# Optimization experiments

Measured on AMD Instinct MI355X. Metric: run time of the kernel, lower is better.

The kernel has to match this reference:

```python
import jax, jax.numpy as jnp
import numpy as np

D_MODEL = 1024
NUM_HEADS = 16
D_K = D_MODEL // NUM_HEADS
MAX_SEQ_LEN = 2048
THETA = 10000.0


def setup_inputs() -> dict:
    key = jax.random.key(0)
    k0, k1, k2, k3, k4 = jax.random.split(key, 5)
    B, S = 2, 2048
    std = (2.0 / (D_MODEL + D_MODEL)) ** 0.5
    # trunc_normal with std=std*std approximated by normal scaled (same distributional scale)
    w = lambda k: (std * std) * jax.random.truncated_normal(k, -3.0 / std, 3.0 / std, (D_MODEL, D_MODEL), jnp.float32)
    return {
        "in_features": jax.random.normal(k0, (B, S, D_MODEL), jnp.float32),
        "token_positions": jnp.arange(S, dtype=jnp.int32),
        "Wq": w(k1), "Wk": w(k2), "Wv": w(k3), "Wo": w(k4),
    }


def _rope(x, token_positions):
    # x: [B, H, S, d_k]; interleaved even/odd rotation
    freq = 1.0 / jnp.power(THETA, jnp.arange(0, D_K, 2, dtype=jnp.float32) / D_K)
    pos = jnp.arange(MAX_SEQ_LEN, dtype=jnp.float32)
    freqs = jnp.outer(pos, freq)                      # [max_seq, d_k/2]
    cos = jnp.cos(freqs)[token_positions]             # [S, d_k/2]
    sin = jnp.sin(freqs)[token_positions]
    even, odd = x[..., 0::2], x[..., 1::2]
    even_out = even * cos - odd * sin
    odd_out = even * sin + odd * cos
    return jnp.stack([even_out, odd_out], axis=-1).reshape(x.shape)


def reference(in_features, token_positions, Wq, Wk, Wv, Wo):
    B, S, _ = in_features.shape
    split = lambda t: t.reshape(B, S, NUM_HEADS, D_K).transpose(0, 2, 1, 3)  # [B,H,S,d_k]
    q = split(in_features @ Wq.T)
    k = split(in_features @ Wk.T)
    v = split(in_features @ Wv.T)
    q = _rope(q, token_positions)
    k = _rope(k, token_positions)
    score = jnp.einsum('bhqd,bhkd->bhqk', q, k) / jnp.sqrt(jnp.float32(D_K))
    mask = jnp.tril(jnp.ones((S, S), dtype=bool))
    score = jnp.where(mask, score, -jnp.inf)
    attn = jax.nn.softmax(score, axis=-1)
    out = jnp.einsum('bhqk,bhkd->bhqd', attn, v)       # [B,H,S,d_k]
    out = out.transpose(0, 2, 1, 3).reshape(B, S, D_MODEL)
    return out @ Wo.T
```

## Files before the change

kernel.cpp:

```cpp
#include <hip/hip_runtime.h>
#include <stdint.h>


typedef unsigned short u16;
typedef __bf16 bf16x8 __attribute__((ext_vector_type(8)));
typedef float f32x4 __attribute__((ext_vector_type(4)));
typedef u16 u16x4 __attribute__((ext_vector_type(4)));

#define LOG2E 1.44269504088896340736f
#define QSCALE (0.125f * LOG2E)

static __device__ __forceinline__ u16 f2bf(float f) {
  __bf16 b = (__bf16)f;
  return __builtin_bit_cast(u16, b);
}

extern "C" __device__ float __ocml_native_exp2_f32(float);
static __device__ __forceinline__ float fexp2(float x) {
#if __has_builtin(__builtin_amdgcn_exp2f)
  return __builtin_amdgcn_exp2f(x);
#else
  return __ocml_native_exp2_f32(x);
#endif
}

template<bool F32>
static __device__ __forceinline__ bf16x8 load8(const void* p, size_t off) {
  if constexpr (F32) {
    const float* f = (const float*)p + off;
    f32x4 a = *(const f32x4*)f;
    f32x4 b = *(const f32x4*)(f + 4);
    bf16x8 r;
    r[0] = (__bf16)a[0]; r[1] = (__bf16)a[1]; r[2] = (__bf16)a[2]; r[3] = (__bf16)a[3];
    r[4] = (__bf16)b[0]; r[5] = (__bf16)b[1]; r[6] = (__bf16)b[2]; r[7] = (__bf16)b[3];
    return r;
  } else {
    return *(const bf16x8*)((const u16*)p + off);
  }
}

static __device__ __forceinline__ void glds16(const u16* g, u16* l) {
  __builtin_amdgcn_global_load_lds(
      (const __attribute__((address_space(1))) unsigned int*)g,
      (__attribute__((address_space(3))) unsigned int*)l, 16, 0, 0);
}

__global__ void prep_kernel(const float* __restrict__ Wq, const float* __restrict__ Wk,
                            const float* __restrict__ Wv, const float* __restrict__ Wo,
                            u16* __restrict__ wout,
                            const float* __restrict__ x, u16* __restrict__ xout,
                            size_t xn8,
                            const int* __restrict__ tp,
                            float* __restrict__ cosT, float* __restrict__ sinT) {
  const int z = blockIdx.z;
  const int i = blockIdx.x * 256 + threadIdx.x;
  if (z == 4) {
    if (i >= 2048 * 32) return;
    int s = i >> 5, fi = i & 31;
    float p = (float)tp[s];
    float freq = powf(10000.0f, -(float)fi / 32.0f);
    float ang = p * freq;
    cosT[i] = cosf(ang);
    sinT[i] = sinf(ang);
    return;
  }
  const float* src;
  u16* dst;
  size_t off;
  if (z < 4) {
    if (i >= 1024 * 1024 / 8) return;
    src = (z == 0) ? Wq : (z == 1) ? Wk : (z == 2) ? Wv : Wo;
    dst = wout + (size_t)z * 1024 * 1024;
    off = (size_t)i * 8;
  } else {
    size_t gi = (size_t)(z - 5) * (512 * 256) + i;
    if (gi >= xn8) return;
    src = x;
    dst = xout;
    off = gi * 8;
  }
  const float* p = src + off;
  f32x4 a = *(const f32x4*)p;
  f32x4 b = *(const f32x4*)(p + 4);
  bf16x8 r;
  r[0] = (__bf16)a[0]; r[1] = (__bf16)a[1]; r[2] = (__bf16)a[2]; r[3] = (__bf16)a[3];
  r[4] = (__bf16)b[0]; r[5] = (__bf16)b[1]; r[6] = (__bf16)b[2]; r[7] = (__bf16)b[3];
  *(bf16x8*)(dst + off) = r;
}

template<bool AF32, bool BF32>
static __device__ __forceinline__ void gemm128_core(
    const void* __restrict__ A, const void* __restrict__ W,
    u16* As, u16* Bs, int m0, int n0, f32x4 (&acc)[4][4]) {
  const int tid = threadIdx.x;
  const int lane = tid & 63;
  const int wave = tid >> 6;
  const int wr = (wave >> 1) * 64, wc = (wave & 1) * 64;
  const int lr = lane & 15, lg = lane >> 4;
  const int srow = tid >> 3;
  const int scol = ((tid & 7) ^ (srow & 7)) * 8;
  for (int k0 = 0; k0 < 1024; k0 += 64) {
    if constexpr (!AF32 && !BF32) {
      const u16* Ab = (const u16*)A;
      const u16* Wb = (const u16*)W;
      __syncthreads();
#pragma unroll
      for (int i = 0; i < 4; ++i) {
        glds16(Ab + (size_t)(m0 + srow + i * 32) * 1024 + k0 + scol, As + tid * 8 + i * 2048);
        glds16(Wb + (size_t)(n0 + srow + i * 32) * 1024 + k0 + scol, Bs + tid * 8 + i * 2048);
      }
      __syncthreads();
    } else {
      bf16x8 ta[4], tb[4];
#pragma unroll
      for (int i = 0; i < 4; ++i) {
        ta[i] = load8<AF32>(A, (size_t)(m0 + srow + i * 32) * 1024 + k0 + scol);
        tb[i] = load8<BF32>(W, (size_t)(n0 + srow + i * 32) * 1024 + k0 + scol);
      }
      __syncthreads();
#pragma unroll
      for (int i = 0; i < 4; ++i) {
        *(bf16x8*)(As + tid * 8 + i * 2048) = ta[i];
        *(bf16x8*)(Bs + tid * 8 + i * 2048) = tb[i];
      }
      __syncthreads();
    }
#pragma unroll
    for (int kk = 0; kk < 2; ++kk) {
      bf16x8 af[4], bfr[4];
#pragma unroll
      for (int i = 0; i < 4; ++i) {
        const int ga = ((kk * 4 + lg) ^ (lr & 7)) * 8;
        af[i]  = *(const bf16x8*)(As + (wr + i * 16 + lr) * 64 + ga);
        bfr[i] = *(const bf16x8*)(Bs + (wc + i * 16 + lr) * 64 + ga);
      }
#pragma unroll
      for (int i = 0; i < 4; ++i)
#pragma unroll
        for (int j = 0; j < 4; ++j)
          acc[i][j] = __builtin_amdgcn_mfma_f32_16x16x32_bf16(af[i], bfr[j], acc[i][j], 0, 0, 0);
    }
  }
}

template<bool F32>
__global__ __launch_bounds__(256, 3)
void qkv_gemm_kernel(const void* __restrict__ X,
                     const void* __restrict__ Wq, const void* __restrict__ Wk,
                     const void* __restrict__ Wv,
                     const float* __restrict__ cosT, const float* __restrict__ sinT,
                     u16* __restrict__ Qo, u16* __restrict__ Ko, u16* __restrict__ Vto) {
  __shared__ __align__(16) u16 As[128 * 64];
  __shared__ __align__(16) u16 Bs[128 * 64];
  const int z = blockIdx.z;
  const void* W = (z == 0) ? Wq : ((z == 1) ? Wk : Wv);
  const int m0 = blockIdx.x * 128, n0 = blockIdx.y * 128;
  f32x4 acc[4][4] = {};
  gemm128_core<F32, F32>(X, W, As, Bs, m0, n0, acc);
  const int lane = threadIdx.x & 63, wave = threadIdx.x >> 6;
  const int wr = (wave >> 1) * 64, wc = (wave & 1) * 64;
  const int lr = lane & 15, lg = lane >> 4;
  if (z < 2) {
    u16* dst = z ? Ko : Qo;
    const float qs = z ? 1.0f : QSCALE;
    const int parity = lr & 1;
#pragma unroll
    for (int i = 0; i < 4; ++i) {
      const int rb = m0 + wr + i * 16 + lg * 4;
#pragma unroll
      for (int n = 0; n < 4; ++n) {
        const int c = n0 + wc + n * 16 + lr;
        const int hh = c >> 6, d = c & 63;
        const int ifr = d >> 1;
#pragma unroll
        for (int j = 0; j < 4; ++j) {
          const int r = rb + j;
          const int s = r & 2047;
          float v = acc[i][n][j];
          float p = __shfl_xor(v, 1);
          float cs = cosT[s * 32 + ifr];
          float sn = sinT[s * 32 + ifr];
          float res = parity ? (p * sn + v * cs) : (v * cs - p * sn);
          dst[(((size_t)(r >> 11) * 16 + hh) * 2048 + s) * 64 + d] =
              f2bf(res * qs);
        }
      }
    }
  } else {
#pragma unroll
    for (int i = 0; i < 4; ++i) {
      const int s0 = m0 + wr + i * 16 + lg * 4;
      const int bb = s0 >> 11, ss = s0 & 2047;
#pragma unroll
      for (int n = 0; n < 4; ++n) {
        const int c = n0 + wc + n * 16 + lr;
        const int hh = c >> 6, d = c & 63;
        u16x4 pk;
#pragma unroll
        for (int j = 0; j < 4; ++j) pk[j] = f2bf(acc[i][n][j]);
        *(u16x4*)(Vto + (((size_t)bb * 16 + hh) * 64 + d) * 2048 + ss) = pk;
      }
    }
  }
}

template<bool MASKED>
static __device__ __forceinline__ void attn_tile(
    const u16* kb, const u16* vb, int kv0, int qrow,
    const bf16x8 (&qf)[2], u16* Psw,
    f32x4 (&accO)[4], float& m, float& l, int lr, int lg) {
  f32x4 sacc[4] = {};
  __builtin_amdgcn_s_setprio(1);
#pragma unroll
  for (int n = 0; n < 4; ++n)
#pragma unroll
    for (int kk = 0; kk < 2; ++kk) {
      const int gsw = ((((kk << 2) | lg) ^ (lr & 7)) << 3);
      bf16x8 kf = *(const bf16x8*)&kb[(n * 16 + lr) * 64 + gsw];
      sacc[n] = __builtin_amdgcn_mfma_f32_16x16x32_bf16(kf, qf[kk], sacc[n], 0, 0, 0);
    }
  __builtin_amdgcn_s_setprio(0);
  if (MASKED) {
#pragma unroll
    for (int n = 0; n < 4; ++n)
#pragma unroll
      for (int j = 0; j < 4; ++j) {
        const int c = kv0 + n * 16 + lg * 4 + j;
        if (c > qrow) sacc[n][j] = -1e30f;
      }
  }
  float t0 = fmaxf(fmaxf(sacc[0][0], sacc[0][1]), sacc[0][2]);
  float t1 = fmaxf(fmaxf(sacc[0][3], sacc[1][0]), sacc[1][1]);
  float t2 = fmaxf(fmaxf(sacc[1][2], sacc[1][3]), sacc[2][0]);
  float t3 = fmaxf(fmaxf(sacc[2][1], sacc[2][2]), sacc[2][3]);
  float t4 = fmaxf(fmaxf(sacc[3][0], sacc[3][1]), sacc[3][2]);
  float tm = fmaxf(fmaxf(t0, t1), fmaxf(fmaxf(t2, t3), fmaxf(t4, sacc[3][3])));
  tm = fmaxf(tm, __shfl_xor(tm, 16));
  tm = fmaxf(tm, __shfl_xor(tm, 32));

  float ssum = 0.f;
  u16x4 pk[4];
  if (__all(tm <= m + 8.0f)) {
#pragma unroll
    for (int n = 0; n < 4; ++n)
#pragma unroll
      for (int j = 0; j < 4; ++j) {
        float p = fexp2(sacc[n][j] - m);
        ssum += p;
        pk[n][j] = f2bf(p);
      }
    ssum += __shfl_xor(ssum, 16);
    ssum += __shfl_xor(ssum, 32);
    l += ssum;
  } else {
    const float mn = fmaxf(m, tm);
    const float al = fexp2(m - mn);
    m = mn;
#pragma unroll
    for (int n = 0; n < 4; ++n)
#pragma unroll
      for (int j = 0; j < 4; ++j) {
        float p = fexp2(sacc[n][j] - mn);
        ssum += p;
        pk[n][j] = f2bf(p);
      }
    ssum += __shfl_xor(ssum, 16);
    ssum += __shfl_xor(ssum, 32);
    l = l * al + ssum;
#pragma unroll
    for (int n = 0; n < 4; ++n)
#pragma unroll
      for (int j = 0; j < 4; ++j)
        accO[n][j] *= al;
  }
#pragma unroll
  for (int n = 0; n < 4; ++n) {
    const int g = n * 4 + lg;
    const int off = ((((g >> 1) ^ (lr & 7)) << 3) | ((g & 1) << 2));
    *(u16x4*)&Psw[lr * 64 + off] = pk[n];
  }
  __builtin_amdgcn_s_setprio(1);
#pragma unroll
  for (int kk = 0; kk < 2; ++kk) {
    const int po = (((kk * 4 + lg) ^ (lr & 7)) << 3);
    bf16x8 pb = *(const bf16x8*)&Psw[lr * 64 + po];
#pragma unroll
    for (int db = 0; db < 4; ++db) {
      const int gsw = ((((kk << 2) | lg) ^ (lr & 7)) << 3);
      bf16x8 vf = *(const bf16x8*)&vb[(db * 16 + lr) * 64 + gsw];
      accO[db] = __builtin_amdgcn_mfma_f32_16x16x32_bf16(vf, pb, accO[db], 0, 0, 0);
    }
  }
  __builtin_amdgcn_s_setprio(0);
}

__global__ __launch_bounds__(256, 4)
void flash_attn_kernel(const u16* __restrict__ Q, const u16* __restrict__ K,
                       const u16* __restrict__ Vt, u16* __restrict__ O) {
  __shared__ __align__(16) u16 Klds[2][64 * 64];
  __shared__ __align__(16) u16 Vlds[2][64 * 64];
  __shared__ __align__(16) u16 Ps[4][16 * 64];
  const int bh = blockIdx.x;
  const int qcb = 31 - (int)blockIdx.y;
  const int b = bh >> 4, h = bh & 15;
  const int tid = threadIdx.x;
  const int wv = tid >> 6, lane = tid & 63;
  const int lr = lane & 15, lg = lane >> 4;
  const int qbase = qcb * 64 + wv * 16;
  const int qrow = qbase + lr;
  const size_t hb = (size_t)bh * (2048 * 64);
  const u16* Qh = Q + hb;

  const int sgr = ((lane & 7) ^ (lane >> 3)) << 3;
  const int srw = lane >> 3;
  const u16* kp = K + hb + (size_t)(wv * 16 + srw) * 64 + sgr;
  const u16* vp = Vt + hb + (size_t)(wv * 16 + srw) * 2048 + sgr;
  const int ldso = (wv * 16) * 64;
  auto STAGE = [&](const u16* kq, const u16* vq, int bufi) {
    u16* kbd = Klds[bufi] + ldso;
    u16* vbd = Vlds[bufi] + ldso;
    glds16(kq, kbd);
    glds16(kq + 8 * 64, kbd + 8 * 64);
    glds16(vq, vbd);
    glds16(vq + 8 * 2048, vbd + 8 * 64);
  };

  bf16x8 qf[2];
#pragma unroll
  for (int kk = 0; kk < 2; ++kk)
    qf[kk] = *(const bf16x8*)(Qh + (size_t)qrow * 64 + kk * 32 + lg * 8);

  f32x4 accO[4] = {};
  float m = -1e30f, l = 0.f;

  const int nt = qcb + 1;
  STAGE(kp, vp, 0);
  kp += 64 * 64; vp += 64;
  __syncthreads();
  for (int t = 0; t < nt - 1; ++t) {
    STAGE(kp, vp, (t & 1) ^ 1);
    kp += 64 * 64; vp += 64;
    attn_tile<false>(Klds[t & 1], Vlds[t & 1], t * 64, qrow, qf, Ps[wv],
                     accO, m, l, lr, lg);
    __syncthreads();
  }
  attn_tile<true>(Klds[(nt - 1) & 1], Vlds[(nt - 1) & 1], (nt - 1) * 64, qrow,
                  qf, Ps[wv], accO, m, l, lr, lg);

  const float inv = 1.0f / l;
#pragma unroll
  for (int db = 0; db < 4; ++db) {
    u16x4 pk;
#pragma unroll
    for (int j = 0; j < 4; ++j) pk[j] = f2bf(accO[db][j] * inv);
    const int d = db * 16 + lg * 4;
    *(u16x4*)&O[((size_t)(b * 2048 + qrow) * 16 + h) * 64 + d] = pk;
  }
}

template<bool WF32>
__global__ __launch_bounds__(256, 2)
void out_gemm_kernel(const u16* __restrict__ A, const void* __restrict__ W,
                     float* __restrict__ out) {
  __shared__ __align__(16) u16 As[128 * 64];
  __shared__ __align__(16) u16 Bs[128 * 64];
  const int m0 = blockIdx.x * 128, n0 = blockIdx.y * 128;
  f32x4 acc[4][4] = {};
  gemm128_core<false, WF32>(A, W, As, Bs, m0, n0, acc);
  const int lane = threadIdx.x & 63, wave = threadIdx.x >> 6;
  const int wr = (wave >> 1) * 64, wc = (wave & 1) * 64;
  const int lr = lane & 15, lg = lane >> 4;
#pragma unroll
  for (int i = 0; i < 4; ++i)
#pragma unroll
    for (int n = 0; n < 4; ++n) {
      const int c = n0 + wc + n * 16 + lr;
#pragma unroll
      for (int j = 0; j < 4; ++j) {
        const int r = m0 + wr + i * 16 + lg * 4 + j;
        out[(size_t)r * 1024 + c] = acc[i][n][j];
      }
    }
}

extern "C" void kernel_launch(void* const* d_in, const int* in_sizes, int n_in,
                              void* d_out, int out_size, void* d_ws, size_t ws_size,
                              hipStream_t stream) {
  const float* x  = (const float*)d_in[0];
  const int*   tp = (const int*)d_in[1];
  const float* Wq = (const float*)d_in[2];
  const float* Wk = (const float*)d_in[3];
  const float* Wv = (const float*)d_in[4];
  const float* Wo = (const float*)d_in[5];
  float* out = (float*)d_out;
  const int B = in_sizes[0] / (2048 * 1024);
  const size_t xel = (size_t)B * 2048 * 1024;
  const size_t tsz = xel * sizeof(u16);
  const size_t TBL = 2048 * 32 * 2 * sizeof(float);
  u16* Qb = (u16*)d_out;
  u16* Kb = (u16*)((char*)d_out + tsz);
  char* ws = (char*)d_ws;
  u16* Vt = (u16*)(ws);
  u16* Ob = (u16*)(ws + tsz);
  float* cosT = (float*)(ws + 2 * tsz);
  float* sinT = cosT + 2048 * 32;
  u16* Xb  = (u16*)(ws + 2 * tsz + TBL);
  u16* Wb4 = Xb + xel;
  const size_t need = 2 * tsz + TBL + tsz + 4 * (size_t)(1024 * 1024) * sizeof(u16);
  const bool cvt = ws_size >= need;
  const size_t xn8 = xel / 8;
  const int xplanes = (int)((xn8 + 512 * 256 - 1) / (512 * 256));

  if (cvt) {
    prep_kernel<<<dim3(512, 1, 5 + xplanes), dim3(256), 0, stream>>>(
        Wq, Wk, Wv, Wo, Wb4, x, Xb, xn8, tp, cosT, sinT);
    qkv_gemm_kernel<false><<<dim3(B * 16, 8, 3), dim3(256), 0, stream>>>(
        Xb, Wb4, Wb4 + 1024 * 1024, Wb4 + 2 * 1024 * 1024, cosT, sinT, Qb, Kb, Vt);
  } else {
    prep_kernel<<<dim3(512, 1, 5), dim3(256), 0, stream>>>(
        Wq, Wk, Wv, Wo, Wb4, x, Xb, 0, tp, cosT, sinT);
    qkv_gemm_kernel<true><<<dim3(B * 16, 8, 3), dim3(256), 0, stream>>>(
        x, Wq, Wk, Wv, cosT, sinT, Qb, Kb, Vt);
  }
  flash_attn_kernel<<<dim3(B * 16, 32), dim3(256), 0, stream>>>(Qb, Kb, Vt, Ob);
  if (cvt) {
    out_gemm_kernel<false><<<dim3(B * 16, 8), dim3(256), 0, stream>>>(
        Ob, Wb4 + 3 * 1024 * 1024, out);
  } else {
    out_gemm_kernel<true><<<dim3(B * 16, 8), dim3(256), 0, stream>>>(Ob, Wo, out);
  }
}
```

Baseline: 103.2 us.

## Process two 16-row query groups per wave in flash attention

Each wave now handles 32 query rows (two 16-row groups) and the block covers 128 queries. Every K/V fragment loaded from LDS is therefore reused for two MFMAs, and the grid shrinks to 16 query blocks per head. The aim is to halve K/V staging and LDS reads per query and amortise per-tile overhead. In exchange it raises register pressure, gives fewer blocks for the causal load balance, and leaves lower waves idle on the final tile.

```diff
diff --git a/kernel.cpp b/kernel.cpp
--- a/kernel.cpp
+++ b/kernel.cpp
@@ -204,12 +204,59 @@
   }
 }
 
+static __device__ __forceinline__ void softmax_rs(
+    f32x4 (&s)[4], float& m, float& l, f32x4 (&accO)[4], u16x4 (&pk)[4]) {
+  float t0 = fmaxf(fmaxf(s[0][0], s[0][1]), s[0][2]);
+  float t1 = fmaxf(fmaxf(s[0][3], s[1][0]), s[1][1]);
+  float t2 = fmaxf(fmaxf(s[1][2], s[1][3]), s[2][0]);
+  float t3 = fmaxf(fmaxf(s[2][1], s[2][2]), s[2][3]);
+  float t4 = fmaxf(fmaxf(s[3][0], s[3][1]), s[3][2]);
+  float tm = fmaxf(fmaxf(t0, t1), fmaxf(fmaxf(t2, t3), fmaxf(t4, s[3][3])));
+  tm = fmaxf(tm, __shfl_xor(tm, 16));
+  tm = fmaxf(tm, __shfl_xor(tm, 32));
+  float ssum = 0.f;
+  if (__all(tm <= m + 8.0f)) {
+#pragma unroll
+    for (int n = 0; n < 4; ++n)
+#pragma unroll
+      for (int j = 0; j < 4; ++j) {
+        float p = fexp2(s[n][j] - m);
+        ssum += p;
+        pk[n][j] = f2bf(p);
+      }
+    ssum += __shfl_xor(ssum, 16);
+    ssum += __shfl_xor(ssum, 32);
+    l += ssum;
+  } else {
+    const float mn = fmaxf(m, tm);
+    const float al = fexp2(m - mn);
+    m = mn;
+#pragma unroll
+    for (int n = 0; n < 4; ++n)
+#pragma unroll
+      for (int j = 0; j < 4; ++j) {
+        float p = fexp2(s[n][j] - mn);
+        ssum += p;
+        pk[n][j] = f2bf(p);
+      }
+    ssum += __shfl_xor(ssum, 16);
+    ssum += __shfl_xor(ssum, 32);
+    l = l * al + ssum;
+#pragma unroll
+    for (int n = 0; n < 4; ++n)
+#pragma unroll
+      for (int j = 0; j < 4; ++j)
+        accO[n][j] *= al;
+  }
+}
+
 template<bool MASKED>
-static __device__ __forceinline__ void attn_tile(
-    const u16* kb, const u16* vb, int kv0, int qrow,
-    const bf16x8 (&qf)[2], u16* Psw,
-    f32x4 (&accO)[4], float& m, float& l, int lr, int lg) {
-  f32x4 sacc[4] = {};
+static __device__ __forceinline__ void attn_tile2(
+    const u16* kb, const u16* vb, int kv0, int qr0, int qr1,
+    const bf16x8 (&qf0)[2], const bf16x8 (&qf1)[2], u16* Psw,
+    f32x4 (&accO0)[4], f32x4 (&accO1)[4],
+    float& m0, float& l0, float& m1, float& l1, int lr, int lg) {
+  f32x4 s0[4] = {}, s1[4] = {};
   __builtin_amdgcn_s_setprio(1);
 #pragma unroll
   for (int n = 0; n < 4; ++n)
@@ -217,7 +264,8 @@
     for (int kk = 0; kk < 2; ++kk) {
       const int gsw = ((((kk << 2) | lg) ^ (lr & 7)) << 3);
       bf16x8 kf = *(const bf16x8*)&kb[(n * 16 + lr) * 64 + gsw];
-      sacc[n] = __builtin_amdgcn_mfma_f32_16x16x32_bf16(kf, qf[kk], sacc[n], 0, 0, 0);
+      s0[n] = __builtin_amdgcn_mfma_f32_16x16x32_bf16(kf, qf0[kk], s0[n], 0, 0, 0);
+      s1[n] = __builtin_amdgcn_mfma_f32_16x16x32_bf16(kf, qf1[kk], s1[n], 0, 0, 0);
     }
   __builtin_amdgcn_s_setprio(0);
   if (MASKED) {
@@ -226,69 +274,45 @@
 #pragma unroll
       for (int j = 0; j < 4; ++j) {
         const int c = kv0 + n * 16 + lg * 4 + j;
-        if (c > qrow) sacc[n][j] = -1e30f;
-      }
-  }
-  float t0 = fmaxf(fmaxf(sacc[0][0], sacc[0][1]), sacc[0][2]);
-  float t1 = fmaxf(fmaxf(sacc[0][3], sacc[1][0]), sacc[1][1]);
-  float t2 = fmaxf(fmaxf(sacc[1][2], sacc[1][3]), sacc[2][0]);
-  float t3 = fmaxf(fmaxf(sacc[2][1], sacc[2][2]), sacc[2][3]);
-  float t4 = fmaxf(fmaxf(sacc[3][0], sacc[3][1]), sacc[3][2]);
-  float tm = fmaxf(fmaxf(t0, t1), fmaxf(fmaxf(t2, t3), fmaxf(t4, sacc[3][3])));
-  tm = fmaxf(tm, __shfl_xor(tm, 16));
-  tm = fmaxf(tm, __shfl_xor(tm, 32));
-
-  float ssum = 0.f;
-  u16x4 pk[4];
-  if (__all(tm <= m + 8.0f)) {
-#pragma unroll
-    for (int n = 0; n < 4; ++n)
-#pragma unroll
-      for (int j = 0; j < 4; ++j) {
-        float p = fexp2(sacc[n][j] - m);
-        ssum += p;
-        pk[n][j] = f2bf(p);
-      }
-    ssum += __shfl_xor(ssum, 16);
-    ssum += __shfl_xor(ssum, 32);
-    l += ssum;
-  } else {
-    const float mn = fmaxf(m, tm);
-    const float al = fexp2(m - mn);
-    m = mn;
-#pragma unroll
-    for (int n = 0; n < 4; ++n)
-#pragma unroll
-      for (int j = 0; j < 4; ++j) {
-        float p = fexp2(sacc[n][j] - mn);
-        ssum += p;
-        pk[n][j] = f2bf(p);
-      }
-    ssum += __shfl_xor(ssum, 16);
-    ssum += __shfl_xor(ssum, 32);
-    l = l * al + ssum;
-#pragma unroll
-    for (int n = 0; n < 4; ++n)
-#pragma unroll
-      for (int j = 0; j < 4; ++j)
-        accO[n][j] *= al;
-  }
+        if (c > qr0) s0[n][j] = -1e30f;
+        if (c > qr1) s1[n][j] = -1e30f;
+      }
+  }
+  u16x4 pk0[4], pk1[4];
+  softmax_rs(s0, m0, l0, accO0, pk0);
+  softmax_rs(s1, m1, l1, accO1, pk1);
+  bf16x8 pb0[2], pb1[2];
 #pragma unroll
   for (int n = 0; n < 4; ++n) {
     const int g = n * 4 + lg;
     const int off = ((((g >> 1) ^ (lr & 7)) << 3) | ((g & 1) << 2));
-    *(u16x4*)&Psw[lr * 64 + off] = pk[n];
-  }
-  __builtin_amdgcn_s_setprio(1);
+    *(u16x4*)&Psw[lr * 64 + off] = pk0[n];
+  }
 #pragma unroll
   for (int kk = 0; kk < 2; ++kk) {
     const int po = (((kk * 4 + lg) ^ (lr & 7)) << 3);
-    bf16x8 pb = *(const bf16x8*)&Psw[lr * 64 + po];
+    pb0[kk] = *(const bf16x8*)&Psw[lr * 64 + po];
+  }
+#pragma unroll
+  for (int n = 0; n < 4; ++n) {
+    const int g = n * 4 + lg;
+    const int off = ((((g >> 1) ^ (lr & 7)) << 3) | ((g & 1) << 2));
+    *(u16x4*)&Psw[lr * 64 + off] = pk1[n];
+  }
+#pragma unroll
+  for (int kk = 0; kk < 2; ++kk) {
+    const int po = (((kk * 4 + lg) ^ (lr & 7)) << 3);
+    pb1[kk] = *(const bf16x8*)&Psw[lr * 64 + po];
+  }
+  __builtin_amdgcn_s_setprio(1);
+#pragma unroll
+  for (int kk = 0; kk < 2; ++kk) {
+    const int gsw = ((((kk << 2) | lg) ^ (lr & 7)) << 3);
 #pragma unroll
     for (int db = 0; db < 4; ++db) {
-      const int gsw = ((((kk << 2) | lg) ^ (lr & 7)) << 3);
       bf16x8 vf = *(const bf16x8*)&vb[(db * 16 + lr) * 64 + gsw];
-      accO[db] = __builtin_amdgcn_mfma_f32_16x16x32_bf16(vf, pb, accO[db], 0, 0, 0);
+      accO0[db] = __builtin_amdgcn_mfma_f32_16x16x32_bf16(vf, pb0[kk], accO0[db], 0, 0, 0);
+      accO1[db] = __builtin_amdgcn_mfma_f32_16x16x32_bf16(vf, pb1[kk], accO1[db], 0, 0, 0);
     }
   }
   __builtin_amdgcn_s_setprio(0);
@@ -301,13 +325,14 @@
   __shared__ __align__(16) u16 Vlds[2][64 * 64];
   __shared__ __align__(16) u16 Ps[4][16 * 64];
   const int bh = blockIdx.x;
-  const int qcb = 31 - (int)blockIdx.y;
+  const int qcb = 15 - (int)blockIdx.y;
   const int b = bh >> 4, h = bh & 15;
   const int tid = threadIdx.x;
   const int wv = tid >> 6, lane = tid & 63;
   const int lr = lane & 15, lg = lane >> 4;
-  const int qbase = qcb * 64 + wv * 16;
-  const int qrow = qbase + lr;
+  const int qb = qcb * 128 + wv * 32;
+  const int qr0 = qb + lr;
+  const int qr1 = qb + 16 + lr;
   const size_t hb = (size_t)bh * (2048 * 64);
   const u16* Qh = Q + hb;
 
@@ -325,36 +350,51 @@
     glds16(vq + 8 * 2048, vbd + 8 * 64);
   };
 
-  bf16x8 qf[2];
-#pragma unroll
-  for (int kk = 0; kk < 2; ++kk)
-    qf[kk] = *(const bf16x8*)(Qh + (size_t)qrow * 64 + kk * 32 + lg * 8);
-
-  f32x4 accO[4] = {};
-  float m = -1e30f, l = 0.f;
-
-  const int nt = qcb + 1;
+  bf16x8 qf0[2], qf1[2];
+#pragma unroll
+  for (int kk = 0; kk < 2; ++kk) {
+    qf0[kk] = *(const bf16x8*)(Qh + (size_t)qr0 * 64 + kk * 32 + lg * 8);
+    qf1[kk] = *(const bf16x8*)(Qh + (size_t)qr1 * 64 + kk * 32 + lg * 8);
+  }
+
+  f32x4 accO0[4] = {}, accO1[4] = {};
+  float m0 = -1e30f, l0 = 0.f, m1 = -1e30f, l1 = 0.f;
+
+  const int ntb = 2 * qcb + 2;
+  const int ntw = 2 * qcb + (wv >= 2 ? 1 : 0) + 1;
   STAGE(kp, vp, 0);
   kp += 64 * 64; vp += 64;
   __syncthreads();
-  for (int t = 0; t < nt - 1; ++t) {
-    STAGE(kp, vp, (t & 1) ^ 1);
-    kp += 64 * 64; vp += 64;
-    attn_tile<false>(Klds[t & 1], Vlds[t & 1], t * 64, qrow, qf, Ps[wv],
-                     accO, m, l, lr, lg);
+  for (int t = 0; t < ntb; ++t) {
+    if (t + 1 < ntb) {
+      STAGE(kp, vp, (t & 1) ^ 1);
+      kp += 64 * 64; vp += 64;
+    }
+    if (t < ntw) {
+      const u16* kb = Klds[t & 1];
+      const u16* vb = Vlds[t & 1];
+      if (t == ntw - 1)
+        attn_tile2<true>(kb, vb, t * 64, qr0, qr1, qf0, qf1, Ps[wv],
+                         accO0, accO1, m0, l0, m1, l1, lr, lg);
+      else
+        attn_tile2<false>(kb, vb, t * 64, qr0, qr1, qf0, qf1, Ps[wv],
+                          accO0, accO1, m0, l0, m1, l1, lr, lg);
+    }
     __syncthreads();
   }
-  attn_tile<true>(Klds[(nt - 1) & 1], Vlds[(nt - 1) & 1], (nt - 1) * 64, qrow,
-                  qf, Ps[wv], accO, m, l, lr, lg);
-
-  const float inv = 1.0f / l;
+
+  const float inv0 = 1.0f / l0, inv1 = 1.0f / l1;
 #pragma unroll
   for (int db = 0; db < 4; ++db) {
-    u16x4 pk;
-#pragma unroll
-    for (int j = 0; j < 4; ++j) pk[j] = f2bf(accO[db][j] * inv);
+    u16x4 w0, w1;
+#pragma unroll
+    for (int j = 0; j < 4; ++j) {
+      w0[j] = f2bf(accO0[db][j] * inv0);
+      w1[j] = f2bf(accO1[db][j] * inv1);
+    }
     const int d = db * 16 + lg * 4;
-    *(u16x4*)&O[((size_t)(b * 2048 + qrow) * 16 + h) * 64 + d] = pk;
+    *(u16x4*)&O[((size_t)(b * 2048 + qr0) * 16 + h) * 64 + d] = w0;
+    *(u16x4*)&O[((size_t)(b * 2048 + qr1) * 16 + h) * 64 + d] = w1;
   }
 }
 
@@ -422,7 +462,7 @@
     qkv_gemm_kernel<true><<<dim3(B * 16, 8, 3), dim3(256), 0, stream>>>(
         x, Wq, Wk, Wv, cosT, sinT, Qb, Kb, Vt);
   }
-  flash_attn_kernel<<<dim3(B * 16, 32), dim3(256), 0, stream>>>(Qb, Kb, Vt, Ob);
+  flash_attn_kernel<<<dim3(B * 16, 16), dim3(256), 0, stream>>>(Qb, Kb, Vt, Ob);
   if (cvt) {
     out_gemm_kernel<false><<<dim3(B * 16, 8), dim3(256), 0, stream>>>(
         Ob, Wb4 + 3 * 1024 * 1024, out);
```

Result: slower. 130.3 us (+26.2%).
